# Performance work log

Hardware: AMD Instinct MI355X
Metric: run time of the kernel (lower is better)

## Reference

```python
import jax, jax.numpy as jnp
import numpy as np

EPS = 1e-5  # torch GroupNorm default


def setup_inputs() -> dict:
    key = jax.random.key(0)
    k1, k2, k3 = jax.random.split(key, 3)
    bs, l, dim = 16, 2048, 512
    G, varDim, numCodes = 2, 256, 320
    x = jax.random.normal(k1, (bs, l, dim), dtype=jnp.float32)
    # grouped 1x1 Conv1d weight: (groups, out_per_group, in_per_group)
    proj_w = jax.random.normal(k2, (G, varDim, varDim), dtype=jnp.float32) / np.sqrt(varDim)
    gn_weight = jnp.ones((dim,), dtype=jnp.float32)
    gn_bias = jnp.zeros((dim,), dtype=jnp.float32)
    embeddings = 0.01 * jax.random.normal(k3, (numCodes, 1, varDim), dtype=jnp.float32)
    return {"x": x, "proj_w": proj_w, "gn_weight": gn_weight,
            "gn_bias": gn_bias, "embeddings": embeddings}


def reference(x, proj_w, gn_weight, gn_bias, embeddings):
    bs, l, dim = x.shape
    G, varDim, _ = proj_w.shape
    numCodes = embeddings.shape[0]

    # --- projection: grouped 1x1 conv ---
    xg = x.transpose(0, 2, 1).reshape(bs, G, varDim, l)            # (bs,G,v,l)
    ze_g = jnp.einsum('gov,bgvl->bgol', proj_w, xg)                # (bs,G,v,l)

    # --- Fp32GroupNorm over (C/G * L) per group ---
    zf = ze_g.astype(jnp.float32)
    mean = zf.mean(axis=(2, 3), keepdims=True)
    var = zf.var(axis=(2, 3), keepdims=True)
    zn = (zf - mean) * jax.lax.rsqrt(var + EPS)
    ze = zn.reshape(bs, dim, l) * gn_weight[None, :, None] + gn_bias[None, :, None]
    ze = ze.astype(x.dtype)                                        # (bs,dim,l)

    # --- VQ: nearest code per group (argmin of L2 == argmin of sq dist) ---
    z = ze.reshape(bs, G, varDim, l).transpose(0, 3, 1, 2)         # (bs,l,G,v)
    emb = jnp.broadcast_to(embeddings, (numCodes, G, varDim))      # combineGroups expand
    dots = jnp.einsum('blgv,cgv->blgc', z, emb)                    # (bs,l,G,C)
    e2 = jnp.sum(emb * emb, axis=-1)                               # (C,G)
    dist = e2.T[None, None] - 2.0 * dots                           # ||z||^2 dropped: const over C
    idx = jnp.argmin(dist, axis=-1)                                # (bs,l,G)

    # gather codes per group
    zq = jnp.take_along_axis(
        emb.transpose(1, 0, 2)[None, None],                        # (1,1,G,C,v)
        idx[..., None, None], axis=3).squeeze(3)                   # (bs,l,G,v)
    zq = zq.reshape(bs, l, dim)

    # straight-through estimator; output shape (bs, l, dim)
    ze_bld = ze.transpose(0, 2, 1)
    out = jax.lax.stop_gradient(zq) + ze_bld - jax.lax.stop_gradient(ze_bld)
    return out
```

## Files before the change

### kernel.cpp

```cpp
#include <hip/hip_runtime.h>
#include <math.h>

typedef _Float16 half8_t  __attribute__((ext_vector_type(8)));
typedef _Float16 half4_t  __attribute__((ext_vector_type(4)));
typedef float    floatx16 __attribute__((ext_vector_type(16)));

#define BS   16
#define LL   2048
#define DIMC 512
#define NG   2
#define VD   256
#define NC   320
#define NELEM ((double)(VD*LL))

#define GLL(gsrc, ldst) __builtin_amdgcn_global_load_lds( \
    (const __attribute__((address_space(1))) unsigned int*)(gsrc), \
    (__attribute__((address_space(3))) unsigned int*)(ldst), 16, 0, 0)

__global__ void k_prep(const float* __restrict__ W, const float* __restrict__ emb,
                       _Float16* __restrict__ Wimg, _Float16* __restrict__ Eimg,
                       float* __restrict__ e2f)
{
  const int blk = blockIdx.x, t = threadIdx.x;
  if (blk < 64) {
    int base = (blk * 256 + t) * 8;
    int k = base & 255, c = k >> 5, kk = k & 31;
    int row = (base >> 8) & 255, g = base >> 16;
    float4 v0 = *(const float4*)(W + base);
    float4 v1 = *(const float4*)(W + base + 4);
    float vv[8] = {v0.x, v0.y, v0.z, v0.w, v1.x, v1.y, v1.z, v1.w};
    half8_t hh, ll;
    #pragma unroll
    for (int i = 0; i < 8; ++i) {
      float s = vv[i] * 16.0f;
      _Float16 h = (_Float16)s;
      hh[i] = h; ll[i] = (_Float16)(s - (float)h);
    }
    size_t rb = ((size_t)(g * 8 + c) * 256 + row) * 72;
    *(half8_t*)&Wimg[rb + kk]      = hh;
    *(half8_t*)&Wimg[rb + 32 + kk] = ll;
  } else if (blk < 104) {
    int base = ((blk - 64) * 256 + t) * 8;
    int k = base & 255, c = k >> 5, kk = k & 31;
    int code = base >> 8;
    float4 v0 = *(const float4*)(emb + base);
    float4 v1 = *(const float4*)(emb + base + 4);
    float vv[8] = {v0.x, v0.y, v0.z, v0.w, v1.x, v1.y, v1.z, v1.w};
    half8_t hh, ll;
    #pragma unroll
    for (int i = 0; i < 8; ++i) {
      float s = vv[i] * 64.0f;
      _Float16 h = (_Float16)s;
      hh[i] = h; ll[i] = (_Float16)(s - (float)h);
    }
    size_t rb = ((size_t)c * 320 + code) * 72;
    *(half8_t*)&Eimg[rb + kk]      = hh;
    *(half8_t*)&Eimg[rb + 32 + kk] = ll;
  } else {
    int code = (blk - 104) * 256 + t;
    if (code < NC) {
      const float* er = emb + (size_t)code * VD;
      double s[4] = {0.0, 0.0, 0.0, 0.0};
      for (int v = 0; v < VD; v += 16)
        #pragma unroll
        for (int u = 0; u < 4; ++u) {
          float4 e4 = *(const float4*)(er + v + u * 4);
          s[u] += (double)e4.x * e4.x + (double)e4.y * e4.y
                + (double)e4.z * e4.z + (double)e4.w * e4.w;
        }
      e2f[code] = (float)(64.0 * (s[0] + s[1] + s[2] + s[3]));
    }
  }
}

__global__ __launch_bounds__(256, 2) void k_proj(
    const float* __restrict__ x, const _Float16* __restrict__ Wimg,
    float* __restrict__ ze, double* __restrict__ stats)
{
  __shared__ _Float16 Ah[128][72];
  __shared__ _Float16 Bh[256 * 72];

  const int blk = blockIdx.x;
  const int g  = blk & 1;
  const int m0 = (blk >> 1) * 128;
  const int b  = m0 >> 11;
  const int t  = threadIdx.x;
  const int lane = t & 63, w = t >> 6;
  const int col  = lane & 31, hq = lane >> 5;
  const int mw = (w & 1) * 64, nw = (w >> 1) * 128;

  const char* wbase = (const char*)(Wimg + (size_t)g * 8 * 256 * 72);

  floatx16 acc[2][4];
  #pragma unroll
  for (int i = 0; i < 2; ++i)
    #pragma unroll
    for (int j = 0; j < 4; ++j)
      #pragma unroll
      for (int e = 0; e < 16; ++e) acc[i][j][e] = 0.f;

  for (int c = 0; c < 8; ++c) {
    #pragma unroll
    for (int i = 0; i < 4; ++i) {
      int idx = i * 256 + t;
      int row = idx >> 3, kq = idx & 7;
      float4 v = *(const float4*)(x + ((size_t)(m0 + row)) * DIMC + g * VD + c * 32 + kq * 4);
      half4_t hh, ll;
      { _Float16 h = (_Float16)v.x; hh[0] = h; ll[0] = (_Float16)(v.x - (float)h); }
      { _Float16 h = (_Float16)v.y; hh[1] = h; ll[1] = (_Float16)(v.y - (float)h); }
      { _Float16 h = (_Float16)v.z; hh[2] = h; ll[2] = (_Float16)(v.z - (float)h); }
      { _Float16 h = (_Float16)v.w; hh[3] = h; ll[3] = (_Float16)(v.w - (float)h); }
      *(half4_t*)&Ah[row][kq * 4]      = hh;
      *(half4_t*)&Ah[row][32 + kq * 4] = ll;
    }
    {
      const char* wc = wbase + (size_t)c * 256 * 144;
      #pragma unroll
      for (int i = 0; i < 9; ++i) {
        int off = (w * 9 + i) * 1024 + lane * 16;
        GLL(wc + off, (char*)Bh + off);
      }
    }
    __syncthreads();
    #pragma unroll
    for (int ks = 0; ks < 2; ++ks) {
      const int ko = ks * 16 + hq * 8;
      half8_t azh[2], azl[2], bwh[4], bwl[4];
      #pragma unroll
      for (int i = 0; i < 2; ++i) {
        azh[i] = *(const half8_t*)&Ah[mw + i * 32 + col][ko];
        azl[i] = *(const half8_t*)&Ah[mw + i * 32 + col][32 + ko];
      }
      #pragma unroll
      for (int j = 0; j < 4; ++j) {
        bwh[j] = *(const half8_t*)&Bh[(nw + j * 32 + col) * 72 + ko];
        bwl[j] = *(const half8_t*)&Bh[(nw + j * 32 + col) * 72 + 32 + ko];
      }
      #pragma unroll
      for (int mi = 0; mi < 2; ++mi)
        #pragma unroll
        for (int ni = 0; ni < 4; ++ni) {
          acc[mi][ni] = __builtin_amdgcn_mfma_f32_32x32x16_f16(azh[mi], bwh[ni], acc[mi][ni], 0, 0, 0);
          acc[mi][ni] = __builtin_amdgcn_mfma_f32_32x32x16_f16(azh[mi], bwl[ni], acc[mi][ni], 0, 0, 0);
          acc[mi][ni] = __builtin_amdgcn_mfma_f32_32x32x16_f16(azl[mi], bwh[ni], acc[mi][ni], 0, 0, 0);
        }
    }
    __syncthreads();
  }

  double s1 = 0.0, s2 = 0.0;
  #pragma unroll
  for (int mi = 0; mi < 2; ++mi)
    #pragma unroll
    for (int ni = 0; ni < 4; ++ni)
      #pragma unroll
      for (int r = 0; r < 16; ++r) {
        float vv = acc[mi][ni][r] * 0.0625f;
        double d = (double)vv; s1 += d; s2 += d * d;
        int ml = mw + mi * 32 + (r & 3) + 8 * (r >> 2) + 4 * hq;
        int nl = nw + ni * 32 + col;
        ze[((size_t)(m0 + ml)) * DIMC + g * VD + nl] = vv;
      }
  #pragma unroll
  for (int off = 32; off > 0; off >>= 1) {
    s1 += __shfl_down(s1, off);
    s2 += __shfl_down(s2, off);
  }
  if (lane == 0) {
    atomicAdd(&stats[(b * NG + g) * 2 + 0], s1);
    atomicAdd(&stats[(b * NG + g) * 2 + 1], s2);
  }
}

__global__ __launch_bounds__(256, 2) void k_vq(
    float* __restrict__ zio, const float* __restrict__ emb,
    const _Float16* __restrict__ Eimg,
    const float* __restrict__ gnw, const float* __restrict__ gnb,
    const double* __restrict__ stats, const float* __restrict__ e2f)
{
  __shared__ _Float16 Zs[128][72];
  __shared__ _Float16 Es[320 * 72];
  __shared__ float e2sh[NC];
  __shared__ int idxs[128];

  const int blk = blockIdx.x;
  const int g  = blk & 1;
  const int m0 = (blk >> 1) * 128;
  const int b  = m0 >> 11;
  const int t  = threadIdx.x;
  const int lane = t & 63, w = t >> 6;
  const int col  = lane & 31, hq = lane >> 5;

  const int si = b * NG + g;
  double ss1 = stats[2 * si], ss2 = stats[2 * si + 1];
  double mu = ss1 / NELEM, var = ss2 / NELEM - mu * mu;
  const float mean = (float)mu;
  const float rstd = (float)(1.0 / sqrt(var + 1e-5));

  for (int c = t; c < NC; c += 256) e2sh[c] = e2f[c];

  float* zbase = zio + (size_t)m0 * DIMC + g * VD;
  const float* gw = gnw + g * VD;
  const float* gb = gnb + g * VD;

  floatx16 acc[10];
  #pragma unroll
  for (int i = 0; i < 10; ++i)
    #pragma unroll
    for (int e = 0; e < 16; ++e) acc[i][e] = 0.f;

  for (int c = 0; c < 8; ++c) {
    #pragma unroll
    for (int i = 0; i < 4; ++i) {
      int idx = i * 256 + t;
      int row = idx >> 3, kq = idx & 7;
      float4 v  = *(const float4*)(zbase + (size_t)row * DIMC + c * 32 + kq * 4);
      float4 w4 = *(const float4*)(gw + c * 32 + kq * 4);
      float4 b4 = *(const float4*)(gb + c * 32 + kq * 4);
      float zn0 = (v.x - mean) * rstd * w4.x + b4.x;
      float zn1 = (v.y - mean) * rstd * w4.y + b4.y;
      float zn2 = (v.z - mean) * rstd * w4.z + b4.z;
      float zn3 = (v.w - mean) * rstd * w4.w + b4.w;
      half4_t hh, ll;
      { _Float16 h = (_Float16)zn0; hh[0] = h; ll[0] = (_Float16)(zn0 - (float)h); }
      { _Float16 h = (_Float16)zn1; hh[1] = h; ll[1] = (_Float16)(zn1 - (float)h); }
      { _Float16 h = (_Float16)zn2; hh[2] = h; ll[2] = (_Float16)(zn2 - (float)h); }
      { _Float16 h = (_Float16)zn3; hh[3] = h; ll[3] = (_Float16)(zn3 - (float)h); }
      *(half4_t*)&Zs[row][kq * 4]      = hh;
      *(half4_t*)&Zs[row][32 + kq * 4] = ll;
    }
    {
      const char* ec = (const char*)Eimg + (size_t)c * 320 * 144;
      for (int i = w; i < 45; i += 4) {
        int off = i * 1024 + lane * 16;
        GLL(ec + off, (char*)Es + off);
      }
    }
    __syncthreads();
    #pragma unroll
    for (int ks = 0; ks < 2; ++ks) {
      const int ko = ks * 16 + hq * 8;
      half8_t bzh = *(const half8_t*)&Zs[w * 32 + col][ko];
      half8_t bzl = *(const half8_t*)&Zs[w * 32 + col][32 + ko];
      #pragma unroll
      for (int mt = 0; mt < 10; ++mt) {
        half8_t aeh = *(const half8_t*)&Es[(mt * 32 + col) * 72 + ko];
        half8_t ael = *(const half8_t*)&Es[(mt * 32 + col) * 72 + 32 + ko];
        acc[mt] = __builtin_amdgcn_mfma_f32_32x32x16_f16(aeh, bzh, acc[mt], 0, 0, 0);
        acc[mt] = __builtin_amdgcn_mfma_f32_32x32x16_f16(aeh, bzl, acc[mt], 0, 0, 0);
        acc[mt] = __builtin_amdgcn_mfma_f32_32x32x16_f16(ael, bzh, acc[mt], 0, 0, 0);
      }
    }
    __syncthreads();
  }

  float bv = 3.4e38f; int bi = 0x7fffffff;
  #pragma unroll
  for (int mt = 0; mt < 10; ++mt)
    #pragma unroll
    for (int r = 0; r < 16; ++r) {
      int code = mt * 32 + (r & 3) + 8 * (r >> 2) + 4 * hq;
      float d = e2sh[code] - 2.0f * acc[mt][r];
      if (d < bv || (d == bv && code < bi)) { bv = d; bi = code; }
    }
  {
    float ov = __shfl_xor(bv, 32);
    int   oi = __shfl_xor(bi, 32);
    if (ov < bv || (ov == bv && oi < bi)) { bv = ov; bi = oi; }
  }
  if (hq == 0) idxs[w * 32 + col] = bi;
  __syncthreads();

  #pragma unroll
  for (int it = 0; it < 32; ++it) {
    int idx = it * 256 + t;
    int row = idx >> 6, q4 = (idx & 63) * 4;
    int id = idxs[row];
    float4 e4 = *(const float4*)(emb + (size_t)id * VD + q4);
    *(float4*)(zbase + (size_t)row * DIMC + q4) = e4;
  }
}

extern "C" void kernel_launch(void* const* d_in, const int* in_sizes, int n_in,
                              void* d_out, int out_size, void* d_ws, size_t ws_size,
                              hipStream_t stream) {
  const float* x   = (const float*)d_in[0];
  const float* W   = (const float*)d_in[1];
  const float* gnw = (const float*)d_in[2];
  const float* gnb = (const float*)d_in[3];
  const float* emb = (const float*)d_in[4];
  float* out = (float*)d_out;

  double*   stats = (double*)d_ws;
  float*    e2f   = (float*)((char*)d_ws + 512);
  _Float16* Wimg  = (_Float16*)((char*)d_ws + 2048);
  _Float16* Eimg  = (_Float16*)((char*)d_ws + 591872);

  hipMemsetAsync(d_ws, 0, 512, stream);
  k_prep<<<106, 256, 0, stream>>>(W, emb, Wimg, Eimg, e2f);
  k_proj<<<512, 256, 0, stream>>>(x, Wimg, out, stats);
  k_vq<<<512, 256, 0, stream>>>(out, emb, Eimg, gnw, gnb, stats, e2f);
}
```

Before: 199.3 us.

## Retile VQ MFMA as 2x2 warp grid and issue LDS loads before conversion

The VQ kernel's warp tiling moves from one warp per 32 rows over all 10 code tiles to a 2x2 grid: each warp covers 64 rows and 5 code tiles. Each warp therefore reads fewer code-embedding fragments from LDS per MFMA. Because the code dimension is now split across warps, the argmin needs a second reduction through shared memory with an extra barrier. Separately, in both the projection and VQ kernels, the async global-to-LDS loads of the weight and codebook tiles are now issued before the fp32-to-fp16 conversion of the activations, so those loads overlap the conversion.

```diff
diff --git a/kernel.cpp b/kernel.cpp
--- a/kernel.cpp
+++ b/kernel.cpp
@@ -16,6 +16,8 @@
 #define GLL(gsrc, ldst) __builtin_amdgcn_global_load_lds( \
     (const __attribute__((address_space(1))) unsigned int*)(gsrc), \
     (__attribute__((address_space(3))) unsigned int*)(ldst), 16, 0, 0)
+
+#define MFMA32 __builtin_amdgcn_mfma_f32_32x32x16_f16
 
 __global__ void k_prep(const float* __restrict__ W, const float* __restrict__ emb,
                        _Float16* __restrict__ Wimg, _Float16* __restrict__ Eimg,
@@ -100,6 +102,14 @@
       for (int e = 0; e < 16; ++e) acc[i][j][e] = 0.f;
 
   for (int c = 0; c < 8; ++c) {
+    {
+      const char* wc = wbase + (size_t)c * 256 * 144;
+      #pragma unroll
+      for (int i = 0; i < 9; ++i) {
+        int off = (w * 9 + i) * 1024 + lane * 16;
+        GLL(wc + off, (char*)Bh + off);
+      }
+    }
     #pragma unroll
     for (int i = 0; i < 4; ++i) {
       int idx = i * 256 + t;
@@ -113,14 +123,6 @@
       *(half4_t*)&Ah[row][kq * 4]      = hh;
       *(half4_t*)&Ah[row][32 + kq * 4] = ll;
     }
-    {
-      const char* wc = wbase + (size_t)c * 256 * 144;
-      #pragma unroll
-      for (int i = 0; i < 9; ++i) {
-        int off = (w * 9 + i) * 1024 + lane * 16;
-        GLL(wc + off, (char*)Bh + off);
-      }
-    }
     __syncthreads();
     #pragma unroll
     for (int ks = 0; ks < 2; ++ks) {
@@ -140,9 +142,9 @@
       for (int mi = 0; mi < 2; ++mi)
         #pragma unroll
         for (int ni = 0; ni < 4; ++ni) {
-          acc[mi][ni] = __builtin_amdgcn_mfma_f32_32x32x16_f16(azh[mi], bwh[ni], acc[mi][ni], 0, 0, 0);
-          acc[mi][ni] = __builtin_amdgcn_mfma_f32_32x32x16_f16(azh[mi], bwl[ni], acc[mi][ni], 0, 0, 0);
-          acc[mi][ni] = __builtin_amdgcn_mfma_f32_32x32x16_f16(azl[mi], bwh[ni], acc[mi][ni], 0, 0, 0);
+          acc[mi][ni] = MFMA32(azh[mi], bwh[ni], acc[mi][ni], 0, 0, 0);
+          acc[mi][ni] = MFMA32(azh[mi], bwl[ni], acc[mi][ni], 0, 0, 0);
+          acc[mi][ni] = MFMA32(azl[mi], bwh[ni], acc[mi][ni], 0, 0, 0);
         }
     }
     __syncthreads();
@@ -181,7 +183,9 @@
   __shared__ _Float16 Zs[128][72];
   __shared__ _Float16 Es[320 * 72];
   __shared__ float e2sh[NC];
-  __shared__ int idxs[128];
+  __shared__ int   idxs[128];
+  __shared__ float cndv[2][128];
+  __shared__ int   cndi[2][128];
 
   const int blk = blockIdx.x;
   const int g  = blk & 1;
@@ -190,6 +194,8 @@
   const int t  = threadIdx.x;
   const int lane = t & 63, w = t >> 6;
   const int col  = lane & 31, hq = lane >> 5;
+  const int ph = w & 1;
+  const int mh = w >> 1;
 
   const int si = b * NG + g;
   double ss1 = stats[2 * si], ss2 = stats[2 * si + 1];
@@ -203,13 +209,22 @@
   const float* gw = gnw + g * VD;
   const float* gb = gnb + g * VD;
 
-  floatx16 acc[10];
-  #pragma unroll
-  for (int i = 0; i < 10; ++i)
-    #pragma unroll
-    for (int e = 0; e < 16; ++e) acc[i][e] = 0.f;
+  floatx16 acc[5][2];
+  #pragma unroll
+  for (int i = 0; i < 5; ++i)
+    #pragma unroll
+    for (int f = 0; f < 2; ++f)
+      #pragma unroll
+      for (int e = 0; e < 16; ++e) acc[i][f][e] = 0.f;
 
   for (int c = 0; c < 8; ++c) {
+    {
+      const char* ec = (const char*)Eimg + (size_t)c * 320 * 144;
+      for (int i = w; i < 45; i += 4) {
+        int off = i * 1024 + lane * 16;
+        GLL(ec + off, (char*)Es + off);
+      }
+    }
     #pragma unroll
     for (int i = 0; i < 4; ++i) {
       int idx = i * 256 + t;
@@ -229,46 +244,60 @@
       *(half4_t*)&Zs[row][kq * 4]      = hh;
       *(half4_t*)&Zs[row][32 + kq * 4] = ll;
     }
-    {
-      const char* ec = (const char*)Eimg + (size_t)c * 320 * 144;
-      for (int i = w; i < 45; i += 4) {
-        int off = i * 1024 + lane * 16;
-        GLL(ec + off, (char*)Es + off);
-      }
-    }
     __syncthreads();
     #pragma unroll
     for (int ks = 0; ks < 2; ++ks) {
       const int ko = ks * 16 + hq * 8;
-      half8_t bzh = *(const half8_t*)&Zs[w * 32 + col][ko];
-      half8_t bzl = *(const half8_t*)&Zs[w * 32 + col][32 + ko];
-      #pragma unroll
-      for (int mt = 0; mt < 10; ++mt) {
-        half8_t aeh = *(const half8_t*)&Es[(mt * 32 + col) * 72 + ko];
-        half8_t ael = *(const half8_t*)&Es[(mt * 32 + col) * 72 + 32 + ko];
-        acc[mt] = __builtin_amdgcn_mfma_f32_32x32x16_f16(aeh, bzh, acc[mt], 0, 0, 0);
-        acc[mt] = __builtin_amdgcn_mfma_f32_32x32x16_f16(aeh, bzl, acc[mt], 0, 0, 0);
-        acc[mt] = __builtin_amdgcn_mfma_f32_32x32x16_f16(ael, bzh, acc[mt], 0, 0, 0);
+      half8_t bzh[2], bzl[2];
+      #pragma unroll
+      for (int f = 0; f < 2; ++f) {
+        bzh[f] = *(const half8_t*)&Zs[ph * 64 + f * 32 + col][ko];
+        bzl[f] = *(const half8_t*)&Zs[ph * 64 + f * 32 + col][32 + ko];
+      }
+      #pragma unroll
+      for (int mtl = 0; mtl < 5; ++mtl) {
+        const _Float16* erow = &Es[((mh * 5 + mtl) * 32 + col) * 72];
+        half8_t aeh = *(const half8_t*)&erow[ko];
+        half8_t ael = *(const half8_t*)&erow[32 + ko];
+        #pragma unroll
+        for (int f = 0; f < 2; ++f) {
+          acc[mtl][f] = MFMA32(aeh, bzh[f], acc[mtl][f], 0, 0, 0);
+          acc[mtl][f] = MFMA32(aeh, bzl[f], acc[mtl][f], 0, 0, 0);
+          acc[mtl][f] = MFMA32(ael, bzh[f], acc[mtl][f], 0, 0, 0);
+        }
       }
     }
     __syncthreads();
   }
 
-  float bv = 3.4e38f; int bi = 0x7fffffff;
-  #pragma unroll
-  for (int mt = 0; mt < 10; ++mt)
+  float bv0 = 3.4e38f, bv1 = 3.4e38f;
+  int   bi0 = 0x7fffffff, bi1 = 0x7fffffff;
+  #pragma unroll
+  for (int mtl = 0; mtl < 5; ++mtl)
     #pragma unroll
     for (int r = 0; r < 16; ++r) {
-      int code = mt * 32 + (r & 3) + 8 * (r >> 2) + 4 * hq;
-      float d = e2sh[code] - 2.0f * acc[mt][r];
-      if (d < bv || (d == bv && code < bi)) { bv = d; bi = code; }
+      int code = (mh * 5 + mtl) * 32 + (r & 3) + 8 * (r >> 2) + 4 * hq;
+      float d0 = e2sh[code] - 2.0f * acc[mtl][0][r];
+      if (d0 < bv0 || (d0 == bv0 && code < bi0)) { bv0 = d0; bi0 = code; }
+      float d1 = e2sh[code] - 2.0f * acc[mtl][1][r];
+      if (d1 < bv1 || (d1 == bv1 && code < bi1)) { bv1 = d1; bi1 = code; }
     }
   {
-    float ov = __shfl_xor(bv, 32);
-    int   oi = __shfl_xor(bi, 32);
-    if (ov < bv || (ov == bv && oi < bi)) { bv = ov; bi = oi; }
-  }
-  if (hq == 0) idxs[w * 32 + col] = bi;
+    float ov = __shfl_xor(bv0, 32); int oi = __shfl_xor(bi0, 32);
+    if (ov < bv0 || (ov == bv0 && oi < bi0)) { bv0 = ov; bi0 = oi; }
+    ov = __shfl_xor(bv1, 32); oi = __shfl_xor(bi1, 32);
+    if (ov < bv1 || (ov == bv1 && oi < bi1)) { bv1 = ov; bi1 = oi; }
+  }
+  if (hq == 0) {
+    cndv[mh][ph * 64 + col]      = bv0; cndi[mh][ph * 64 + col]      = bi0;
+    cndv[mh][ph * 64 + 32 + col] = bv1; cndi[mh][ph * 64 + 32 + col] = bi1;
+  }
+  __syncthreads();
+  if (t < 128) {
+    float v0 = cndv[0][t], v1 = cndv[1][t];
+    int   i0 = cndi[0][t], i1 = cndi[1][t];
+    idxs[t] = (v1 < v0 || (v1 == v0 && i1 < i0)) ? i1 : i0;
+  }
   __syncthreads();
 
   #pragma unroll
```

After: 197.0 us. Within noise of the previous version (-1.2%).

## Restructure VQ loop over code tiles with Z in registers and double-buffered codebook

Applied to the files above, without the earlier changes.

k_vq now normalizes and converts all of its Z tile into registers first, with double-buffered LDS staging. It then loops over 32-code tiles of a re-laid-out codebook image, prefetching the next tile with global_load_lds while computing the current one. This keeps one accumulator instead of ten and streams the codebook with overlap, at the cost of many live half8 registers (zfh/zfl). k_proj gets register prefetch of the next x chunk to overlap global loads with MFMA, and the stats memset is folded into k_prep to drop a launch.

```diff
diff --git a/kernel.cpp b/kernel.cpp
--- a/kernel.cpp
+++ b/kernel.cpp
@@ -17,9 +17,11 @@
     (const __attribute__((address_space(1))) unsigned int*)(gsrc), \
     (__attribute__((address_space(3))) unsigned int*)(ldst), 16, 0, 0)
 
+#define MFMA32 __builtin_amdgcn_mfma_f32_32x32x16_f16
+
 __global__ void k_prep(const float* __restrict__ W, const float* __restrict__ emb,
                        _Float16* __restrict__ Wimg, _Float16* __restrict__ Eimg,
-                       float* __restrict__ e2f)
+                       float* __restrict__ e2f, double* __restrict__ stats)
 {
   const int blk = blockIdx.x, t = threadIdx.x;
   if (blk < 64) {
@@ -43,6 +45,7 @@
     int base = ((blk - 64) * 256 + t) * 8;
     int k = base & 255, c = k >> 5, kk = k & 31;
     int code = base >> 8;
+    int mt = code >> 5, cl = code & 31;
     float4 v0 = *(const float4*)(emb + base);
     float4 v1 = *(const float4*)(emb + base + 4);
     float vv[8] = {v0.x, v0.y, v0.z, v0.w, v1.x, v1.y, v1.z, v1.w};
@@ -53,7 +56,7 @@
       _Float16 h = (_Float16)s;
       hh[i] = h; ll[i] = (_Float16)(s - (float)h);
     }
-    size_t rb = ((size_t)c * 320 + code) * 72;
+    size_t rb = ((size_t)((mt * 8 + c) * 32 + cl)) * 72;
     *(half8_t*)&Eimg[rb + kk]      = hh;
     *(half8_t*)&Eimg[rb + 32 + kk] = ll;
   } else {
@@ -70,6 +73,7 @@
         }
       e2f[code] = (float)(64.0 * (s[0] + s[1] + s[2] + s[3]));
     }
+    if (blk == 105 && t >= 64 && t < 128) stats[t - 64] = 0.0;
   }
 }
 
@@ -88,8 +92,10 @@
   const int lane = t & 63, w = t >> 6;
   const int col  = lane & 31, hq = lane >> 5;
   const int mw = (w & 1) * 64, nw = (w >> 1) * 128;
+  const int rw = t >> 3, kq = t & 7;
 
   const char* wbase = (const char*)(Wimg + (size_t)g * 8 * 256 * 72);
+  const float* xrow = x + (size_t)m0 * DIMC + g * VD + kq * 4;
 
   floatx16 acc[2][4];
   #pragma unroll
@@ -99,20 +105,12 @@
       #pragma unroll
       for (int e = 0; e < 16; ++e) acc[i][j][e] = 0.f;
 
+  float4 xv[4];
+  #pragma unroll
+  for (int i = 0; i < 4; ++i)
+    xv[i] = *(const float4*)(xrow + (size_t)(i * 32 + rw) * DIMC);
+
   for (int c = 0; c < 8; ++c) {
-    #pragma unroll
-    for (int i = 0; i < 4; ++i) {
-      int idx = i * 256 + t;
-      int row = idx >> 3, kq = idx & 7;
-      float4 v = *(const float4*)(x + ((size_t)(m0 + row)) * DIMC + g * VD + c * 32 + kq * 4);
-      half4_t hh, ll;
-      { _Float16 h = (_Float16)v.x; hh[0] = h; ll[0] = (_Float16)(v.x - (float)h); }
-      { _Float16 h = (_Float16)v.y; hh[1] = h; ll[1] = (_Float16)(v.y - (float)h); }
-      { _Float16 h = (_Float16)v.z; hh[2] = h; ll[2] = (_Float16)(v.z - (float)h); }
-      { _Float16 h = (_Float16)v.w; hh[3] = h; ll[3] = (_Float16)(v.w - (float)h); }
-      *(half4_t*)&Ah[row][kq * 4]      = hh;
-      *(half4_t*)&Ah[row][32 + kq * 4] = ll;
-    }
     {
       const char* wc = wbase + (size_t)c * 256 * 144;
       #pragma unroll
@@ -121,7 +119,23 @@
         GLL(wc + off, (char*)Bh + off);
       }
     }
+    #pragma unroll
+    for (int i = 0; i < 4; ++i) {
+      int row = i * 32 + rw;
+      half4_t hh, ll;
+      { _Float16 h = (_Float16)xv[i].x; hh[0] = h; ll[0] = (_Float16)(xv[i].x - (float)h); }
+      { _Float16 h = (_Float16)xv[i].y; hh[1] = h; ll[1] = (_Float16)(xv[i].y - (float)h); }
+      { _Float16 h = (_Float16)xv[i].z; hh[2] = h; ll[2] = (_Float16)(xv[i].z - (float)h); }
+      { _Float16 h = (_Float16)xv[i].w; hh[3] = h; ll[3] = (_Float16)(xv[i].w - (float)h); }
+      *(half4_t*)&Ah[row][kq * 4]      = hh;
+      *(half4_t*)&Ah[row][32 + kq * 4] = ll;
+    }
     __syncthreads();
+    if (c < 7) {
+      #pragma unroll
+      for (int i = 0; i < 4; ++i)
+        xv[i] = *(const float4*)(xrow + (size_t)(i * 32 + rw) * DIMC + (c + 1) * 32);
+    }
     #pragma unroll
     for (int ks = 0; ks < 2; ++ks) {
       const int ko = ks * 16 + hq * 8;
@@ -140,9 +154,9 @@
       for (int mi = 0; mi < 2; ++mi)
         #pragma unroll
         for (int ni = 0; ni < 4; ++ni) {
-          acc[mi][ni] = __builtin_amdgcn_mfma_f32_32x32x16_f16(azh[mi], bwh[ni], acc[mi][ni], 0, 0, 0);
-          acc[mi][ni] = __builtin_amdgcn_mfma_f32_32x32x16_f16(azh[mi], bwl[ni], acc[mi][ni], 0, 0, 0);
-          acc[mi][ni] = __builtin_amdgcn_mfma_f32_32x32x16_f16(azl[mi], bwh[ni], acc[mi][ni], 0, 0, 0);
+          acc[mi][ni] = MFMA32(azh[mi], bwh[ni], acc[mi][ni], 0, 0, 0);
+          acc[mi][ni] = MFMA32(azh[mi], bwl[ni], acc[mi][ni], 0, 0, 0);
+          acc[mi][ni] = MFMA32(azl[mi], bwh[ni], acc[mi][ni], 0, 0, 0);
         }
     }
     __syncthreads();
@@ -178,10 +192,14 @@
     const float* __restrict__ gnw, const float* __restrict__ gnb,
     const double* __restrict__ stats, const float* __restrict__ e2f)
 {
-  __shared__ _Float16 Zs[128][72];
-  __shared__ _Float16 Es[320 * 72];
+  __shared__ __align__(16) _Float16 smem[36864];
   __shared__ float e2sh[NC];
-  __shared__ int idxs[128];
+  __shared__ int   idxs[128];
+
+  _Float16* const Zs0 = smem;
+  _Float16* const Zs1 = smem + 9216;
+  _Float16* const EsA = smem;
+  _Float16* const EsB = smem + 18432;
 
   const int blk = blockIdx.x;
   const int g  = blk & 1;
@@ -190,6 +208,7 @@
   const int t  = threadIdx.x;
   const int lane = t & 63, w = t >> 6;
   const int col  = lane & 31, hq = lane >> 5;
+  const int rw = t >> 3, kq = t & 7;
 
   const int si = b * NG + g;
   double ss1 = stats[2 * si], ss2 = stats[2 * si + 1];
@@ -197,26 +216,29 @@
   const float mean = (float)mu;
   const float rstd = (float)(1.0 / sqrt(var + 1e-5));
 
-  for (int c = t; c < NC; c += 256) e2sh[c] = e2f[c];
+  for (int cc = t; cc < NC; cc += 256) e2sh[cc] = e2f[cc];
 
   float* zbase = zio + (size_t)m0 * DIMC + g * VD;
   const float* gw = gnw + g * VD;
   const float* gb = gnb + g * VD;
 
-  floatx16 acc[10];
-  #pragma unroll
-  for (int i = 0; i < 10; ++i)
-    #pragma unroll
-    for (int e = 0; e < 16; ++e) acc[i][e] = 0.f;
-
-  for (int c = 0; c < 8; ++c) {
+  half8_t zfh[8][2], zfl[8][2];
+
+  {
+    const char* ec = (const char*)Eimg;
+    #pragma unroll
+    for (int i = 0; i < 9; ++i) {
+      int off = (w * 9 + i) * 1024 + lane * 16;
+      GLL(ec + off, (char*)EsB + off);
+    }
+  }
+  {
+    float4 w4 = *(const float4*)(gw + kq * 4);
+    float4 b4 = *(const float4*)(gb + kq * 4);
     #pragma unroll
     for (int i = 0; i < 4; ++i) {
-      int idx = i * 256 + t;
-      int row = idx >> 3, kq = idx & 7;
-      float4 v  = *(const float4*)(zbase + (size_t)row * DIMC + c * 32 + kq * 4);
-      float4 w4 = *(const float4*)(gw + c * 32 + kq * 4);
-      float4 b4 = *(const float4*)(gb + c * 32 + kq * 4);
+      int row = i * 32 + rw;
+      float4 v = *(const float4*)(zbase + (size_t)row * DIMC + kq * 4);
       float zn0 = (v.x - mean) * rstd * w4.x + b4.x;
       float zn1 = (v.y - mean) * rstd * w4.y + b4.y;
       float zn2 = (v.z - mean) * rstd * w4.z + b4.z;
@@ -226,43 +248,89 @@
       { _Float16 h = (_Float16)zn1; hh[1] = h; ll[1] = (_Float16)(zn1 - (float)h); }
       { _Float16 h = (_Float16)zn2; hh[2] = h; ll[2] = (_Float16)(zn2 - (float)h); }
       { _Float16 h = (_Float16)zn3; hh[3] = h; ll[3] = (_Float16)(zn3 - (float)h); }
-      *(half4_t*)&Zs[row][kq * 4]      = hh;
-      *(half4_t*)&Zs[row][32 + kq * 4] = ll;
-    }
+      *(half4_t*)&Zs0[row * 72 + kq * 4]      = hh;
+      *(half4_t*)&Zs0[row * 72 + 32 + kq * 4] = ll;
+    }
+  }
+  #pragma unroll
+  for (int c = 1; c < 8; ++c) {
+    __syncthreads();
+    float4 zv[4];
+    float4 w4 = *(const float4*)(gw + c * 32 + kq * 4);
+    float4 b4 = *(const float4*)(gb + c * 32 + kq * 4);
+    #pragma unroll
+    for (int i = 0; i < 4; ++i)
+      zv[i] = *(const float4*)(zbase + (size_t)(i * 32 + rw) * DIMC + c * 32 + kq * 4);
     {
-      const char* ec = (const char*)Eimg + (size_t)c * 320 * 144;
-      for (int i = w; i < 45; i += 4) {
-        int off = i * 1024 + lane * 16;
-        GLL(ec + off, (char*)Es + off);
-      }
-    }
+      const _Float16* Zr = ((c - 1) & 1) ? Zs1 : Zs0;
+      #pragma unroll
+      for (int ks = 0; ks < 2; ++ks) {
+        const int ko = ks * 16 + hq * 8;
+        zfh[c - 1][ks] = *(const half8_t*)&Zr[(w * 32 + col) * 72 + ko];
+        zfl[c - 1][ks] = *(const half8_t*)&Zr[(w * 32 + col) * 72 + 32 + ko];
+      }
+    }
+    {
+      _Float16* Zw = (c & 1) ? Zs1 : Zs0;
+      #pragma unroll
+      for (int i = 0; i < 4; ++i) {
+        int row = i * 32 + rw;
+        float zn0 = (zv[i].x - mean) * rstd * w4.x + b4.x;
+        float zn1 = (zv[i].y - mean) * rstd * w4.y + b4.y;
+        float zn2 = (zv[i].z - mean) * rstd * w4.z + b4.z;
+        float zn3 = (zv[i].w - mean) * rstd * w4.w + b4.w;
+        half4_t hh, ll;
+        { _Float16 h = (_Float16)zn0; hh[0] = h; ll[0] = (_Float16)(zn0 - (float)h); }
+        { _Float16 h = (_Float16)zn1; hh[1] = h; ll[1] = (_Float16)(zn1 - (float)h); }
+        { _Float16 h = (_Float16)zn2; hh[2] = h; ll[2] = (_Float16)(zn2 - (float)h); }
+        { _Float16 h = (_Float16)zn3; hh[3] = h; ll[3] = (_Float16)(zn3 - (float)h); }
+        *(half4_t*)&Zw[row * 72 + kq * 4]      = hh;
+        *(half4_t*)&Zw[row * 72 + 32 + kq * 4] = ll;
+      }
+    }
+  }
+  __syncthreads();
+  #pragma unroll
+  for (int ks = 0; ks < 2; ++ks) {
+    const int ko = ks * 16 + hq * 8;
+    zfh[7][ks] = *(const half8_t*)&Zs1[(w * 32 + col) * 72 + ko];
+    zfl[7][ks] = *(const half8_t*)&Zs1[(w * 32 + col) * 72 + 32 + ko];
+  }
+
+  float bv = 3.4e38f; int bi = 0x7fffffff;
+  for (int mt = 0; mt < 10; ++mt) {
+    const _Float16* Eb = (mt & 1) ? EsA : EsB;
     __syncthreads();
-    #pragma unroll
-    for (int ks = 0; ks < 2; ++ks) {
-      const int ko = ks * 16 + hq * 8;
-      half8_t bzh = *(const half8_t*)&Zs[w * 32 + col][ko];
-      half8_t bzl = *(const half8_t*)&Zs[w * 32 + col][32 + ko];
-      #pragma unroll
-      for (int mt = 0; mt < 10; ++mt) {
-        half8_t aeh = *(const half8_t*)&Es[(mt * 32 + col) * 72 + ko];
-        half8_t ael = *(const half8_t*)&Es[(mt * 32 + col) * 72 + 32 + ko];
-        acc[mt] = __builtin_amdgcn_mfma_f32_32x32x16_f16(aeh, bzh, acc[mt], 0, 0, 0);
-        acc[mt] = __builtin_amdgcn_mfma_f32_32x32x16_f16(aeh, bzl, acc[mt], 0, 0, 0);
-        acc[mt] = __builtin_amdgcn_mfma_f32_32x32x16_f16(ael, bzh, acc[mt], 0, 0, 0);
-      }
-    }
-    __syncthreads();
-  }
-
-  float bv = 3.4e38f; int bi = 0x7fffffff;
-  #pragma unroll
-  for (int mt = 0; mt < 10; ++mt)
+    if (mt < 9) {
+      const char* ec = (const char*)Eimg + (size_t)(mt + 1) * 36864;
+      char* eb = (mt & 1) ? (char*)EsB : (char*)EsA;
+      #pragma unroll
+      for (int i = 0; i < 9; ++i) {
+        int off = (w * 9 + i) * 1024 + lane * 16;
+        GLL(ec + off, eb + off);
+      }
+    }
+    floatx16 vacc;
+    #pragma unroll
+    for (int e = 0; e < 16; ++e) vacc[e] = 0.f;
+    #pragma unroll
+    for (int c = 0; c < 8; ++c)
+      #pragma unroll
+      for (int ks = 0; ks < 2; ++ks) {
+        const int ko = ks * 16 + hq * 8;
+        half8_t aeh = *(const half8_t*)&Eb[(c * 32 + col) * 72 + ko];
+        half8_t ael = *(const half8_t*)&Eb[(c * 32 + col) * 72 + 32 + ko];
+        vacc = MFMA32(aeh, zfh[c][ks], vacc, 0, 0, 0);
+        vacc = MFMA32(aeh, zfl[c][ks], vacc, 0, 0, 0);
+        vacc = MFMA32(ael, zfh[c][ks], vacc, 0, 0, 0);
+      }
     #pragma unroll
     for (int r = 0; r < 16; ++r) {
       int code = mt * 32 + (r & 3) + 8 * (r >> 2) + 4 * hq;
-      float d = e2sh[code] - 2.0f * acc[mt][r];
+      float d = e2sh[code] - 2.0f * vacc[r];
       if (d < bv || (d == bv && code < bi)) { bv = d; bi = code; }
     }
+  }
   {
     float ov = __shfl_xor(bv, 32);
     int   oi = __shfl_xor(bi, 32);
@@ -296,8 +364,7 @@
   _Float16* Wimg  = (_Float16*)((char*)d_ws + 2048);
   _Float16* Eimg  = (_Float16*)((char*)d_ws + 591872);
 
-  hipMemsetAsync(d_ws, 0, 512, stream);
-  k_prep<<<106, 256, 0, stream>>>(W, emb, Wimg, Eimg, e2f);
+  k_prep<<<106, 256, 0, stream>>>(W, emb, Wimg, Eimg, e2f, stats);
   k_proj<<<512, 256, 0, stream>>>(x, Wimg, out, stats);
   k_vq<<<512, 256, 0, stream>>>(out, emb, Eimg, gnw, gnb, stats, e2f);
 }
```

Result: no change. 198.0 us (-0.7%).
